# Kernel tuning notes

Measured on AMD Instinct MI355X. Metric: run time of the kernel, lower is better.

## Reference

```python
import jax, jax.numpy as jnp
import numpy as np

N = 16384; E = 262144; G = 32; NPG = N // G
D_FEAT = 256; AA_DIM = 64; N_LABELS = 21
H0, O0 = 2, 64      # layer0: in 320 -> 2 heads x 64, flatten -> 128
H1, O1 = 2, 256     # out layer: in 128 -> 2 heads x 256, mean over heads -> 256
NCLS = 2
NEG_SLOPE = 0.2     # DGL GATConv LeakyReLU default


def setup_inputs() -> dict:
    key = jax.random.key(0)
    ks = jax.random.split(key, 32)

    def gn(k, shape, fan):
        return jax.random.normal(k, shape, dtype=jnp.float32) / np.float32(np.sqrt(fan))

    din0 = AA_DIM + D_FEAT
    din1 = H0 * O0
    inp = {}
    inp['feat'] = jax.random.normal(ks[0], (N, D_FEAT), dtype=jnp.float32)
    inp['aa_emb'] = gn(ks[1], (N_LABELS, AA_DIM), 1.0)
    inp['W0'] = gn(ks[2], (din0, H0 * O0), din0)
    inp['al0'] = gn(ks[3], (H0, O0), O0)
    inp['ar0'] = gn(ks[4], (H0, O0), O0)
    inp['res0'] = gn(ks[5], (din0, H0 * O0), din0)
    inp['b0'] = jnp.zeros((H0 * O0,), jnp.float32)
    inp['W1'] = gn(ks[6], (din1, H1 * O1), din1)
    inp['al1'] = gn(ks[7], (H1, O1), O1)
    inp['ar1'] = gn(ks[8], (H1, O1), O1)
    inp['res1'] = gn(ks[9], (din1, H1 * O1), din1)
    inp['b1'] = jnp.zeros((H1 * O1,), jnp.float32)
    inp['mW0'] = gn(ks[10], (O1, O1 // 2), O1)
    inp['mb0'] = jnp.zeros((O1 // 2,), jnp.float32)
    inp['mW1'] = gn(ks[11], (O1 // 2, O1 // 4), O1 // 2)
    inp['mb1'] = jnp.zeros((O1 // 4,), jnp.float32)
    inp['mW2'] = gn(ks[12], (O1 // 4, NCLS), O1 // 4)
    inp['mb2'] = jnp.zeros((NCLS,), jnp.float32)
    inp['ref_aa'] = jax.random.randint(ks[13], (N,), 0, N_LABELS)
    inp['alt_aa'] = jax.random.randint(ks[14], (G,), 0, N_LABELS)
    inp['src'] = jax.random.randint(ks[15], (E,), 0, N)
    inp['dst'] = jax.random.randint(ks[16], (E,), 0, N)
    inp['graph_id'] = jnp.arange(N) // NPG   # 512 nodes per graph, contiguous
    return inp


def _gat_conv(h, src, dst, W, al, ar, resW, bias, heads, out, act):
    n = h.shape[0]
    ft = (h @ W).reshape(n, heads, out)                # [N,H,O] projected src/dst feats
    el = jnp.einsum('nho,ho->nh', ft, al)
    er = jnp.einsum('nho,ho->nh', ft, ar)
    e = el[src] + er[dst]                              # [E,H]
    e = jnp.where(e > 0, e, NEG_SLOPE * e)             # LeakyReLU
    # edge softmax over incoming edges of each dst node
    emax = jax.ops.segment_max(e, dst, num_segments=n)
    ez = jnp.exp(e - emax[dst])
    denom = jax.ops.segment_sum(ez, dst, num_segments=n)
    alpha = ez / denom[dst]                            # [E,H]
    rst = jax.ops.segment_sum(ft[src] * alpha[:, :, None], dst, num_segments=n)
    rst = rst + (h @ resW).reshape(n, heads, out) + bias.reshape(1, heads, out)
    return act(rst) if act is not None else rst


def _forward(feat, aa_emb, W0, al0, ar0, res0, b0, W1, al1, ar1, res1, b1,
             mW0, mb0, mW1, mb1, mW2, mb2, ref_aa, alt_aa, src, dst, graph_id):
    # per-node ref amino-acid embedding gated by per-graph alt embedding
    h_aa = aa_emb[ref_aa] * aa_emb[alt_aa][graph_id]   # [N, AA_DIM]
    h = jnp.concatenate([h_aa, feat], axis=-1)         # [N, 320]
    h = _gat_conv(h, src, dst, W0, al0, ar0, res0, b0, H0, O0, jax.nn.elu).reshape(N, -1)
    h = _gat_conv(h, src, dst, W1, al1, ar1, res1, b1, H1, O1, None)   # [N,H1,O1]
    h = jax.nn.elu(jnp.mean(h, axis=1))                # mean over heads -> [N, O1]
    hg = jax.ops.segment_sum(h, graph_id, num_segments=G) / np.float32(NPG)  # mean readout
    x = jnp.maximum(hg @ mW0 + mb0, 0.0)               # MLPReadout (L=2, ReLU)
    x = jnp.maximum(x @ mW1 + mb1, 0.0)
    return x @ mW2 + mb2                               # [G, NCLS] logits


def reference(feat, aa_emb, W0, al0, ar0, res0, b0, W1, al1, ar1, res1, b1,
              mW0, mb0, mW1, mb1, mW2, mb2, ref_aa, alt_aa, src, dst, graph_id):
    return _forward(feat, aa_emb, W0, al0, ar0, res0, b0, W1, al1, ar1, res1, b1,
                    mW0, mb0, mW1, mb1, mW2, mb2, ref_aa, alt_aa, src, dst, graph_id)
```

## Files before the change

### kernel.cpp

```cpp
#include <hip/hip_runtime.h>
#include <hip/hip_bf16.h>

#define NN 16384
#define EE 262144
#define GG 32
#define NPGC 512
#define NEG_SLOPE 0.2f

typedef __attribute__((ext_vector_type(8))) short bf16x8;
typedef __attribute__((ext_vector_type(4))) float f32x4;

__device__ __forceinline__ float b2f(short s) {
    union { float f; unsigned u; } c;
    c.u = ((unsigned)(unsigned short)s) << 16;
    return c.f;
}

__device__ __forceinline__ short f2b(float f) {
    __hip_bfloat16 b = __float2bfloat16(f);
    short r;
    __builtin_memcpy(&r, &b, 2);
    return r;
}

__global__ __launch_bounds__(320) void prep_kernel(
    const float* __restrict__ feat, const float* __restrict__ aa_emb,
    const int* __restrict__ ref_aa, const int* __restrict__ alt_aa,
    const int* __restrict__ graph_id, __hip_bfloat16* __restrict__ h,
    int* __restrict__ deg,
    const float* __restrict__ W0, const float* __restrict__ R0,
    const float* __restrict__ W1, const float* __restrict__ R1,
    __hip_bfloat16* __restrict__ wt0, __hip_bfloat16* __restrict__ wt1)
{
    int b = blockIdx.x, t = threadIdx.x;
    if (b < NN) {
        int n = b;
        if (t == 0) deg[n] = 0;
        float v;
        if (t < 64) {
            int ra = ref_aa[n], ga = alt_aa[graph_id[n]];
            v = aa_emb[ra * 64 + t] * aa_emb[ga * 64 + t];
        } else {
            v = feat[(size_t)n * 256 + (t - 64)];
        }
        h[(size_t)n * 320 + t] = __float2bfloat16(v);
    } else if (b < NN + 256) {
        int c = b - NN;
        float v = (c < 128) ? W0[(size_t)t * 128 + c] : R0[(size_t)t * 128 + (c - 128)];
        wt0[(size_t)c * 320 + t] = __float2bfloat16(v);
    } else {
        int cc = b - NN - 256;
        if (t < 128) {
            float v = (cc < 512) ? W1[(size_t)t * 512 + cc] : R1[(size_t)t * 512 + (cc - 512)];
            wt1[(size_t)cc * 128 + t] = __float2bfloat16(v);
        }
    }
}

template<int FR, int C1, int KTOT>
__device__ __forceinline__ void gemm_body(
    const __hip_bfloat16* __restrict__ A, const __hip_bfloat16* __restrict__ Bt,
    __hip_bfloat16* __restrict__ ftb, __hip_bfloat16* __restrict__ resb,
    int bx, int by, short* lds)
{
    constexpr int BM = 32 * FR;
    short* As = lds;
    short* Bs = lds + BM * 64;
    int t = threadIdx.x;
    int wid = t >> 6, lane = t & 63;
    int wr = wid >> 1, wc = wid & 1;
    int row0 = bx * BM, col0 = by * BM;

    f32x4 acc[FR][FR];
#pragma unroll
    for (int m = 0; m < FR; m++)
#pragma unroll
        for (int n = 0; n < FR; n++) acc[m][n] = (f32x4){0.f, 0.f, 0.f, 0.f};

    for (int kk = 0; kk < KTOT; kk += 64) {
        __syncthreads();
#pragma unroll
        for (int c = t; c < BM * 8; c += 256) {
            int row = c >> 3, slot = c & 7;
            int sw = (slot ^ (row & 7)) * 8;
            bf16x8 va = *(const bf16x8*)(A + (size_t)(row0 + row) * KTOT + kk + slot * 8);
            *(bf16x8*)(&As[row * 64 + sw]) = va;
            bf16x8 vb = *(const bf16x8*)(Bt + (size_t)(col0 + row) * KTOT + kk + slot * 8);
            *(bf16x8*)(&Bs[row * 64 + sw]) = vb;
        }
        __syncthreads();
#pragma unroll
        for (int ks = 0; ks < 2; ks++) {
            int kslot = ks * 4 + (lane >> 4);
            bf16x8 a[FR], bfr[FR];
#pragma unroll
            for (int m = 0; m < FR; m++) {
                int row = wr * FR * 16 + m * 16 + (lane & 15);
                a[m] = *(const bf16x8*)(&As[row * 64 + ((kslot ^ (row & 7)) * 8)]);
            }
#pragma unroll
            for (int n = 0; n < FR; n++) {
                int col = wc * FR * 16 + n * 16 + (lane & 15);
                bfr[n] = *(const bf16x8*)(&Bs[col * 64 + ((kslot ^ (col & 7)) * 8)]);
            }
#pragma unroll
            for (int m = 0; m < FR; m++)
#pragma unroll
                for (int n = 0; n < FR; n++)
                    acc[m][n] = __builtin_amdgcn_mfma_f32_16x16x32_bf16(a[m], bfr[n], acc[m][n], 0, 0, 0);
        }
    }

#pragma unroll
    for (int m = 0; m < FR; m++)
#pragma unroll
        for (int n = 0; n < FR; n++) {
            int colg = col0 + wc * FR * 16 + n * 16 + (lane & 15);
            int rbase = row0 + wr * FR * 16 + m * 16 + (lane >> 4) * 4;
#pragma unroll
            for (int r = 0; r < 4; r++) {
                float v = acc[m][n][r];
                int rg = rbase + r;
                if (colg < C1) ftb[(size_t)rg * C1 + colg] = __float2bfloat16(v);
                else           resb[(size_t)rg * C1 + (colg - C1)] = __float2bfloat16(v);
            }
        }
}

__global__ __launch_bounds__(256) void gemm0_deg_kernel(
    const __hip_bfloat16* __restrict__ A, const __hip_bfloat16* __restrict__ Bt,
    __hip_bfloat16* __restrict__ ftb, __hip_bfloat16* __restrict__ resb,
    const int* __restrict__ dst, int* __restrict__ deg)
{
    __shared__ short lds[2 * 64 * 64];
    int b = blockIdx.x;
    if (b < 1024) {
        gemm_body<2, 128, 320>(A, Bt, ftb, resb, b & 255, b >> 8, lds);
    } else {
        int i = (b - 1024) * 256 + threadIdx.x;
        if (i < EE) atomicAdd(&deg[dst[i]], 1);
    }
}

__global__ __launch_bounds__(256) void gemm1_kernel(
    const __hip_bfloat16* __restrict__ A, const __hip_bfloat16* __restrict__ Bt,
    __hip_bfloat16* __restrict__ ftb, __hip_bfloat16* __restrict__ resb)
{
    __shared__ short lds[2 * 128 * 64];
    gemm_body<4, 512, 128>(A, Bt, ftb, resb, blockIdx.x, blockIdx.y, lds);
}

__global__ __launch_bounds__(256) void scan_elr0_kernel(
    const int* __restrict__ deg, int* __restrict__ row, int* __restrict__ cursor,
    const __hip_bfloat16* __restrict__ ftb,
    const float* __restrict__ al, const float* __restrict__ ar,
    float* __restrict__ el, float* __restrict__ er)
{
    int b = blockIdx.x, t = threadIdx.x;
    if (b == 0) {
        __shared__ int part[256];
        __shared__ int pref[257];
        int base = t * 64;
        int s = 0;
        for (int i = 0; i < 64; i++) s += deg[base + i];
        part[t] = s;
        __syncthreads();
        if (t == 0) {
            int a = 0;
            for (int i = 0; i < 256; i++) { pref[i] = a; a += part[i]; }
            pref[256] = a;
        }
        __syncthreads();
        int a = pref[t];
        for (int i = 0; i < 64; i++) {
            row[base + i] = a; cursor[base + i] = a;
            a += deg[base + i];
        }
        if (t == 0) row[NN] = pref[256];
    } else {
        int gid = (b - 1) * 256 + t;
        int wv = gid >> 6, lane = gid & 63;
        int n = wv >> 1, hh = wv & 1;
        if (n >= NN) return;
        float f = b2f(((const short*)ftb)[(size_t)n * 128 + hh * 64 + lane]);
        float sl = f * al[hh * 64 + lane];
        float sr = f * ar[hh * 64 + lane];
#pragma unroll
        for (int d = 32; d; d >>= 1) { sl += __shfl_xor(sl, d); sr += __shfl_xor(sr, d); }
        if (lane == 0) { el[n * 2 + hh] = sl; er[n * 2 + hh] = sr; }
    }
}

__global__ __launch_bounds__(256) void scatter_kernel(
    const int* __restrict__ src, const int* __restrict__ dst,
    int* __restrict__ cursor, int* __restrict__ srcs)
{
    int i = blockIdx.x * 256 + threadIdx.x;
    if (i < EE) {
        int p = atomicAdd(&cursor[dst[i]], 1);
        srcs[p] = src[i];
    }
}

__global__ __launch_bounds__(256) void elr1_kernel(
    const __hip_bfloat16* __restrict__ ftb,
    const float* __restrict__ al, const float* __restrict__ ar,
    float* __restrict__ el, float* __restrict__ er)
{
    int wv = (blockIdx.x * 256 + threadIdx.x) >> 6;
    int lane = threadIdx.x & 63;
    if (wv >= NN) return;
    int n = wv, hh = lane >> 5, dim = lane * 8;
    bf16x8 v = *(const bf16x8*)((const short*)ftb + (size_t)n * 512 + dim);
    float sl = 0.f, sr = 0.f;
#pragma unroll
    for (int j = 0; j < 8; j++) {
        float f = b2f(v[j]);
        sl += f * al[dim + j];
        sr += f * ar[dim + j];
    }
#pragma unroll
    for (int d = 16; d; d >>= 1) { sl += __shfl_xor(sl, d); sr += __shfl_xor(sr, d); }
    if ((lane & 31) == 0) { el[n * 2 + hh] = sl; er[n * 2 + hh] = sr; }
}

__global__ __launch_bounds__(256) void agg0_kernel(
    const __hip_bfloat16* __restrict__ ftb0, const __hip_bfloat16* __restrict__ resb0,
    const int* __restrict__ row, const int* __restrict__ srcs,
    const float* __restrict__ el, const float* __restrict__ er,
    const float* __restrict__ b0, __hip_bfloat16* __restrict__ h1)
{
    int wv = (blockIdx.x * 256 + threadIdx.x) >> 6;
    int lane = threadIdx.x & 63;
    if (wv >= NN) return;
    int n = wv;
    int eo = lane >> 4, vo = lane & 15;
    int hh = vo >> 3, dim = vo * 8;
    int e0 = row[n], e1 = row[n + 1];
    float er0v = er[n * 2 + 0], er1v = er[n * 2 + 1];

    float acc[8] = {0.f, 0.f, 0.f, 0.f, 0.f, 0.f, 0.f, 0.f};
    float ts0 = 0.f, ts1 = 0.f;
    for (int base = e0; base < e1; base += 64) {
        int c = min(64, e1 - base);
        float w0 = 0.f, w1 = 0.f;
        int sm = -1;
        if (lane < c) {
            sm = srcs[base + lane];
            float v0 = el[sm * 2 + 0] + er0v; v0 = v0 > 0.f ? v0 : NEG_SLOPE * v0;
            float v1 = el[sm * 2 + 1] + er1v; v1 = v1 > 0.f ? v1 : NEG_SLOPE * v1;
            w0 = __expf(v0); w1 = __expf(v1);
        }
        ts0 += w0; ts1 += w1;
        for (int i = eo; i < c; i += 4) {
            int s = __shfl(sm, i);
            float a0 = __shfl(w0, i), a1 = __shfl(w1, i);
            float a = hh ? a1 : a0;
            bf16x8 v = *(const bf16x8*)((const short*)ftb0 + (size_t)s * 128 + dim);
#pragma unroll
            for (int j = 0; j < 8; j++) acc[j] += a * b2f(v[j]);
        }
    }
#pragma unroll
    for (int d = 32; d; d >>= 1) { ts0 += __shfl_xor(ts0, d); ts1 += __shfl_xor(ts1, d); }
#pragma unroll
    for (int j = 0; j < 8; j++) acc[j] += __shfl_xor(acc[j], 16);
#pragma unroll
    for (int j = 0; j < 8; j++) acc[j] += __shfl_xor(acc[j], 32);
    if (eo == 0) {
        float s = hh ? ts1 : ts0;
        float invv = s > 0.f ? 1.f / s : 0.f;
        bf16x8 res = *(const bf16x8*)((const short*)resb0 + (size_t)n * 128 + dim);
        bf16x8 o;
#pragma unroll
        for (int j = 0; j < 8; j++) {
            float r = acc[j] * invv + b2f(res[j]) + b0[dim + j];
            r = r > 0.f ? r : (__expf(r) - 1.f);
            o[j] = f2b(r);
        }
        *(bf16x8*)((short*)h1 + (size_t)n * 128 + dim) = o;
    }
}

__global__ __launch_bounds__(256) void agg1_kernel(
    const __hip_bfloat16* __restrict__ ftb1, const __hip_bfloat16* __restrict__ resb1,
    const int* __restrict__ row, const int* __restrict__ srcs,
    const float* __restrict__ el, const float* __restrict__ er,
    const float* __restrict__ b1, float* __restrict__ part)
{
    __shared__ float red[4][256];
    int t = threadIdx.x;
    int lane = t & 63, wid = t >> 6;
    int n = blockIdx.x * 4 + wid;
    int hh = lane >> 5, dim = lane * 8;
    int e0 = row[n], e1 = row[n + 1];
    float er0v = er[n * 2 + 0], er1v = er[n * 2 + 1];

    float acc[8] = {0.f, 0.f, 0.f, 0.f, 0.f, 0.f, 0.f, 0.f};
    float ts0 = 0.f, ts1 = 0.f;
    for (int base = e0; base < e1; base += 64) {
        int c = min(64, e1 - base);
        float w0 = 0.f, w1 = 0.f;
        int sm = -1;
        if (lane < c) {
            sm = srcs[base + lane];
            float v0 = el[sm * 2 + 0] + er0v; v0 = v0 > 0.f ? v0 : NEG_SLOPE * v0;
            float v1 = el[sm * 2 + 1] + er1v; v1 = v1 > 0.f ? v1 : NEG_SLOPE * v1;
            w0 = __expf(v0); w1 = __expf(v1);
        }
        ts0 += w0; ts1 += w1;
        int i = 0;
        for (; i + 4 <= c; i += 4) {
            int sA = __shfl(sm, i),     sB = __shfl(sm, i + 1);
            int sC = __shfl(sm, i + 2), sD = __shfl(sm, i + 3);
            float a0A = __shfl(w0, i),     a1A = __shfl(w1, i);
            float a0B = __shfl(w0, i + 1), a1B = __shfl(w1, i + 1);
            float a0C = __shfl(w0, i + 2), a1C = __shfl(w1, i + 2);
            float a0D = __shfl(w0, i + 3), a1D = __shfl(w1, i + 3);
            float aA = hh ? a1A : a0A, aB = hh ? a1B : a0B;
            float aC = hh ? a1C : a0C, aD = hh ? a1D : a0D;
            bf16x8 vA = *(const bf16x8*)((const short*)ftb1 + (size_t)sA * 512 + dim);
            bf16x8 vB = *(const bf16x8*)((const short*)ftb1 + (size_t)sB * 512 + dim);
            bf16x8 vC = *(const bf16x8*)((const short*)ftb1 + (size_t)sC * 512 + dim);
            bf16x8 vD = *(const bf16x8*)((const short*)ftb1 + (size_t)sD * 512 + dim);
#pragma unroll
            for (int j = 0; j < 8; j++) {
                acc[j] += aA * b2f(vA[j]) + aB * b2f(vB[j]) + aC * b2f(vC[j]) + aD * b2f(vD[j]);
            }
        }
        for (; i < c; i++) {
            int s = __shfl(sm, i);
            float a0 = __shfl(w0, i), a1 = __shfl(w1, i);
            float a = hh ? a1 : a0;
            bf16x8 v = *(const bf16x8*)((const short*)ftb1 + (size_t)s * 512 + dim);
#pragma unroll
            for (int j = 0; j < 8; j++) acc[j] += a * b2f(v[j]);
        }
    }
#pragma unroll
    for (int d = 32; d; d >>= 1) { ts0 += __shfl_xor(ts0, d); ts1 += __shfl_xor(ts1, d); }
    float s = hh ? ts1 : ts0;
    float invv = s > 0.f ? 1.f / s : 0.f;

    bf16x8 res = *(const bf16x8*)((const short*)resb1 + (size_t)n * 512 + dim);
    float r[8];
#pragma unroll
    for (int j = 0; j < 8; j++)
        r[j] = acc[j] * invv + b2f(res[j]) + b1[dim + j];
    float v[8];
#pragma unroll
    for (int j = 0; j < 8; j++) {
        float o = __shfl_xor(r[j], 32);
        v[j] = 0.5f * (r[j] + o);
    }
    if (lane < 32) {
#pragma unroll
        for (int j = 0; j < 8; j++) {
            float x = v[j];
            x = x > 0.f ? x : (__expf(x) - 1.f);
            red[wid][lane * 8 + j] = x;
        }
    }
    __syncthreads();
    part[(size_t)blockIdx.x * 256 + t] = red[0][t] + red[1][t] + red[2][t] + red[3][t];
}

__global__ __launch_bounds__(256) void readout2_kernel(
    const float* __restrict__ part,
    const float* __restrict__ mW0, const float* __restrict__ mb0,
    const float* __restrict__ mW1, const float* __restrict__ mb1,
    const float* __restrict__ mW2, const float* __restrict__ mb2,
    float* __restrict__ out)
{
    __shared__ float hg[256];
    __shared__ float x1[128];
    __shared__ float x2[64];
    int g = blockIdx.x, t = threadIdx.x;
    float s = 0.f;
    for (int c = 0; c < 128; c++) s += part[(size_t)(g * 128 + c) * 256 + t];
    hg[t] = s * (1.f / (float)NPGC);
    __syncthreads();
    if (t < 128) {
        float a = mb0[t];
        for (int k = 0; k < 256; k++) a += hg[k] * mW0[k * 128 + t];
        x1[t] = fmaxf(a, 0.f);
    }
    __syncthreads();
    if (t < 64) {
        float a = mb1[t];
        for (int k = 0; k < 128; k++) a += x1[k] * mW1[k * 64 + t];
        x2[t] = fmaxf(a, 0.f);
    }
    __syncthreads();
    if (t < 2) {
        float a = mb2[t];
        for (int k = 0; k < 64; k++) a += x2[k] * mW2[k * 2 + t];
        out[g * 2 + t] = a;
    }
}

extern "C" void kernel_launch(void* const* d_in, const int* in_sizes, int n_in,
                              void* d_out, int out_size, void* d_ws, size_t ws_size,
                              hipStream_t stream)
{
    const float* feat   = (const float*)d_in[0];
    const float* aa_emb = (const float*)d_in[1];
    const float* W0     = (const float*)d_in[2];
    const float* al0    = (const float*)d_in[3];
    const float* ar0    = (const float*)d_in[4];
    const float* res0   = (const float*)d_in[5];
    const float* b0     = (const float*)d_in[6];
    const float* W1     = (const float*)d_in[7];
    const float* al1    = (const float*)d_in[8];
    const float* ar1    = (const float*)d_in[9];
    const float* res1   = (const float*)d_in[10];
    const float* b1     = (const float*)d_in[11];
    const float* mW0    = (const float*)d_in[12];
    const float* mb0    = (const float*)d_in[13];
    const float* mW1    = (const float*)d_in[14];
    const float* mb1    = (const float*)d_in[15];
    const float* mW2    = (const float*)d_in[16];
    const float* mb2    = (const float*)d_in[17];
    const int* ref_aa   = (const int*)d_in[18];
    const int* alt_aa   = (const int*)d_in[19];
    const int* src      = (const int*)d_in[20];
    const int* dst      = (const int*)d_in[21];
    const int* graph_id = (const int*)d_in[22];
    float* out = (float*)d_out;

    size_t off = 0;
    auto alloc = [&](size_t bytes) -> void* {
        void* p = (char*)d_ws + off;
        off += (bytes + 255) & ~(size_t)255;
        return p;
    };
    __hip_bfloat16* h     = (__hip_bfloat16*)alloc((size_t)NN * 320 * 2);
    __hip_bfloat16* wt0   = (__hip_bfloat16*)alloc((size_t)256 * 320 * 2);
    __hip_bfloat16* wt1   = (__hip_bfloat16*)alloc((size_t)1024 * 128 * 2);
    __hip_bfloat16* ftb0  = (__hip_bfloat16*)alloc((size_t)NN * 128 * 2);
    __hip_bfloat16* resb0 = (__hip_bfloat16*)alloc((size_t)NN * 128 * 2);
    __hip_bfloat16* h1b   = (__hip_bfloat16*)alloc((size_t)NN * 128 * 2);
    __hip_bfloat16* ftb1  = (__hip_bfloat16*)alloc((size_t)NN * 512 * 2);
    __hip_bfloat16* resb1 = (__hip_bfloat16*)alloc((size_t)NN * 512 * 2);
    float* el0    = (float*)alloc((size_t)NN * 2 * 4);
    float* er0    = (float*)alloc((size_t)NN * 2 * 4);
    float* el1    = (float*)alloc((size_t)NN * 2 * 4);
    float* er1    = (float*)alloc((size_t)NN * 2 * 4);
    int* deg      = (int*)alloc((size_t)NN * 4);
    int* row      = (int*)alloc((size_t)(NN + 1) * 4);
    int* cursor   = (int*)alloc((size_t)NN * 4);
    int* srcs     = (int*)alloc((size_t)EE * 4);
    float* part   = (float*)alloc((size_t)(NN / 4) * 256 * 4);

    (void)in_sizes; (void)n_in; (void)out_size; (void)ws_size;

    prep_kernel<<<NN + 256 + 1024, 320, 0, stream>>>(
        feat, aa_emb, ref_aa, alt_aa, graph_id, h, deg, W0, res0, W1, res1, wt0, wt1);
    gemm0_deg_kernel<<<2048, 256, 0, stream>>>(h, wt0, ftb0, resb0, dst, deg);
    scan_elr0_kernel<<<1 + 8192, 256, 0, stream>>>(deg, row, cursor, ftb0, al0, ar0, el0, er0);
    scatter_kernel<<<EE / 256, 256, 0, stream>>>(src, dst, cursor, srcs);
    agg0_kernel<<<NN / 4, 256, 0, stream>>>(ftb0, resb0, row, srcs, el0, er0, b0, h1b);
    gemm1_kernel<<<dim3(128, 8), 256, 0, stream>>>(h1b, wt1, ftb1, resb1);
    elr1_kernel<<<NN / 4, 256, 0, stream>>>(ftb1, al1, ar1, el1, er1);
    agg1_kernel<<<NN / 4, 256, 0, stream>>>(ftb1, resb1, row, srcs, el1, er1, b1, part);
    readout2_kernel<<<GG, 256, 0, stream>>>(part, mW0, mb0, mW1, mb1, mW2, mb2, out);
}
```

Before: 148.3 us.

## Fold layer-1 attention vectors into weights and compute el/er in agg0 epilogue

Precomputes W1·al1 and W1·ar1 (128x2 each) in one extra prep block, then computes layer-1 attention logits directly from the fp32 layer-0 output inside the agg0 epilogue. This removes the elr1 kernel launch and its full read of the 16 MB bf16 ftb1 buffer. The single prep block runs a serial 256-long loop per thread, which could lengthen prep. Numerics shift slightly because logits now come from fp32 h1 rather than bf16-rounded projections.

```diff
diff --git a/kernel.cpp b/kernel.cpp
--- a/kernel.cpp
+++ b/kernel.cpp
@@ -30,7 +30,9 @@
     int* __restrict__ deg,
     const float* __restrict__ W0, const float* __restrict__ R0,
     const float* __restrict__ W1, const float* __restrict__ R1,
-    __hip_bfloat16* __restrict__ wt0, __hip_bfloat16* __restrict__ wt1)
+    __hip_bfloat16* __restrict__ wt0, __hip_bfloat16* __restrict__ wt1,
+    const float* __restrict__ al1, const float* __restrict__ ar1,
+    float* __restrict__ wal1, float* __restrict__ war1)
 {
     int b = blockIdx.x, t = threadIdx.x;
     if (b < NN) {
@@ -48,11 +50,24 @@
         int c = b - NN;
         float v = (c < 128) ? W0[(size_t)t * 128 + c] : R0[(size_t)t * 128 + (c - 128)];
         wt0[(size_t)c * 320 + t] = __float2bfloat16(v);
-    } else {
+    } else if (b < NN + 256 + 1024) {
         int cc = b - NN - 256;
         if (t < 128) {
             float v = (cc < 512) ? W1[(size_t)t * 512 + cc] : R1[(size_t)t * 512 + (cc - 512)];
             wt1[(size_t)cc * 128 + t] = __float2bfloat16(v);
+        }
+    } else {
+        if (t < 128) {
+            for (int hh = 0; hh < 2; hh++) {
+                float sl = 0.f, sr = 0.f;
+                for (int o = 0; o < 256; o++) {
+                    float w = W1[(size_t)t * 512 + hh * 256 + o];
+                    sl += w * al1[hh * 256 + o];
+                    sr += w * ar1[hh * 256 + o];
+                }
+                wal1[t * 2 + hh] = sl;
+                war1[t * 2 + hh] = sr;
+            }
         }
     }
 }
@@ -202,33 +217,13 @@
     }
 }
 
-__global__ __launch_bounds__(256) void elr1_kernel(
-    const __hip_bfloat16* __restrict__ ftb,
-    const float* __restrict__ al, const float* __restrict__ ar,
-    float* __restrict__ el, float* __restrict__ er)
-{
-    int wv = (blockIdx.x * 256 + threadIdx.x) >> 6;
-    int lane = threadIdx.x & 63;
-    if (wv >= NN) return;
-    int n = wv, hh = lane >> 5, dim = lane * 8;
-    bf16x8 v = *(const bf16x8*)((const short*)ftb + (size_t)n * 512 + dim);
-    float sl = 0.f, sr = 0.f;
-#pragma unroll
-    for (int j = 0; j < 8; j++) {
-        float f = b2f(v[j]);
-        sl += f * al[dim + j];
-        sr += f * ar[dim + j];
-    }
-#pragma unroll
-    for (int d = 16; d; d >>= 1) { sl += __shfl_xor(sl, d); sr += __shfl_xor(sr, d); }
-    if ((lane & 31) == 0) { el[n * 2 + hh] = sl; er[n * 2 + hh] = sr; }
-}
-
 __global__ __launch_bounds__(256) void agg0_kernel(
     const __hip_bfloat16* __restrict__ ftb0, const __hip_bfloat16* __restrict__ resb0,
     const int* __restrict__ row, const int* __restrict__ srcs,
     const float* __restrict__ el, const float* __restrict__ er,
-    const float* __restrict__ b0, __hip_bfloat16* __restrict__ h1)
+    const float* __restrict__ b0, __hip_bfloat16* __restrict__ h1,
+    const float* __restrict__ wal1, const float* __restrict__ war1,
+    float* __restrict__ el1, float* __restrict__ er1)
 {
     int wv = (blockIdx.x * 256 + threadIdx.x) >> 6;
     int lane = threadIdx.x & 63;
@@ -272,13 +267,33 @@
         float invv = s > 0.f ? 1.f / s : 0.f;
         bf16x8 res = *(const bf16x8*)((const short*)resb0 + (size_t)n * 128 + dim);
         bf16x8 o;
+        float rr[8];
 #pragma unroll
         for (int j = 0; j < 8; j++) {
             float r = acc[j] * invv + b2f(res[j]) + b0[dim + j];
             r = r > 0.f ? r : (__expf(r) - 1.f);
+            rr[j] = r;
             o[j] = f2b(r);
         }
         *(bf16x8*)((short*)h1 + (size_t)n * 128 + dim) = o;
+
+        float pl0 = 0.f, pl1 = 0.f, pr0 = 0.f, pr1 = 0.f;
+#pragma unroll
+        for (int j = 0; j < 8; j++) {
+            float x = rr[j];
+            int k = dim + j;
+            pl0 += x * wal1[k * 2 + 0]; pl1 += x * wal1[k * 2 + 1];
+            pr0 += x * war1[k * 2 + 0]; pr1 += x * war1[k * 2 + 1];
+        }
+#pragma unroll
+        for (int d = 1; d <= 8; d <<= 1) {
+            pl0 += __shfl_xor(pl0, d); pl1 += __shfl_xor(pl1, d);
+            pr0 += __shfl_xor(pr0, d); pr1 += __shfl_xor(pr1, d);
+        }
+        if (vo == 0) {
+            el1[n * 2 + 0] = pl0; el1[n * 2 + 1] = pl1;
+            er1[n * 2 + 0] = pr0; er1[n * 2 + 1] = pr1;
+        }
     }
 }
 
@@ -446,6 +461,8 @@
     float* er0    = (float*)alloc((size_t)NN * 2 * 4);
     float* el1    = (float*)alloc((size_t)NN * 2 * 4);
     float* er1    = (float*)alloc((size_t)NN * 2 * 4);
+    float* wal1   = (float*)alloc((size_t)128 * 2 * 4);
+    float* war1   = (float*)alloc((size_t)128 * 2 * 4);
     int* deg      = (int*)alloc((size_t)NN * 4);
     int* row      = (int*)alloc((size_t)(NN + 1) * 4);
     int* cursor   = (int*)alloc((size_t)NN * 4);
@@ -454,14 +471,15 @@
 
     (void)in_sizes; (void)n_in; (void)out_size; (void)ws_size;
 
-    prep_kernel<<<NN + 256 + 1024, 320, 0, stream>>>(
-        feat, aa_emb, ref_aa, alt_aa, graph_id, h, deg, W0, res0, W1, res1, wt0, wt1);
+    prep_kernel<<<NN + 256 + 1024 + 1, 320, 0, stream>>>(
+        feat, aa_emb, ref_aa, alt_aa, graph_id, h, deg, W0, res0, W1, res1, wt0, wt1,
+        al1, ar1, wal1, war1);
     gemm0_deg_kernel<<<2048, 256, 0, stream>>>(h, wt0, ftb0, resb0, dst, deg);
     scan_elr0_kernel<<<1 + 8192, 256, 0, stream>>>(deg, row, cursor, ftb0, al0, ar0, el0, er0);
     scatter_kernel<<<EE / 256, 256, 0, stream>>>(src, dst, cursor, srcs);
-    agg0_kernel<<<NN / 4, 256, 0, stream>>>(ftb0, resb0, row, srcs, el0, er0, b0, h1b);
+    agg0_kernel<<<NN / 4, 256, 0, stream>>>(
+        ftb0, resb0, row, srcs, el0, er0, b0, h1b, wal1, war1, el1, er1);
     gemm1_kernel<<<dim3(128, 8), 256, 0, stream>>>(h1b, wt1, ftb1, resb1);
-    elr1_kernel<<<NN / 4, 256, 0, stream>>>(ftb1, al1, ar1, el1, er1);
     agg1_kernel<<<NN / 4, 256, 0, stream>>>(ftb1, resb1, row, srcs, el1, er1, b1, part);
     readout2_kernel<<<GG, 256, 0, stream>>>(part, mW0, mb0, mW1, mb1, mW2, mb2, out);
 }
```

New measurement: 166.2 us. +12.1%, slower.
